# Kernel optimization log

Measured on AMD Instinct MI355X. Metric: run time of the kernel, lower is better.

## Reference

```python
import jax, jax.numpy as jnp
import numpy as np

B, S, D, R, N, K = 4, 2048, 1024, 128, 64, 8

def _orthogonal(key, shape):
    # mimic nn.init.orthogonal_ for a (D, R) matrix, D >= R
    a = jax.random.normal(key, (shape[0], shape[1]), dtype=jnp.float32)
    q, r = jnp.linalg.qr(a)
    q = q * jnp.sign(jnp.diagonal(r))[None, :]
    return q

def setup_inputs() -> dict:
    key = jax.random.key(0)
    kx, kr, kn = jax.random.split(key, 3)
    x = jax.random.normal(kx, (B, S, D), dtype=jnp.float32)
    # router: nn.Linear(d_model, n_compress, bias=False) -> weight [N, D]
    bound = 1.0 / np.sqrt(D)
    router_w = jax.random.uniform(kr, (N, D), minval=-bound, maxval=bound, dtype=jnp.float32)
    # compress_neurons: [N, D, R], each slice orthogonally initialized
    nkeys = jax.random.split(kn, N)
    neurons = jax.vmap(lambda k: _orthogonal(k, (D, R)))(nkeys)  # [N, D, R]
    return {"x": x, "router_w": router_w, "neurons": neurons}

def reference(x, router_w, neurons):
    # scores: [B, S, N]
    scores = jnp.einsum('bsd,nd->bsn', x, router_w)
    topk_scores, topk_idx = jax.lax.top_k(scores, K)           # [B,S,K]
    weights = jax.nn.softmax(topk_scores, axis=-1)             # [B,S,K]
    # Equivalent to gathering per-token [K,D,R] expert matrices then bmm,
    # but computed as dense all-expert projection + gather (no [B,S,K,D,R] blow-up).
    proj_all = jnp.einsum('bsd,ndr->bsnr', x, neurons)         # [B,S,N,R]
    proj = jnp.take_along_axis(proj_all, topk_idx[..., None], axis=2)  # [B,S,K,R]
    output = jnp.sum(proj * weights[..., None], axis=2)        # [B,S,R]
    return output, weights, topk_idx
```

## Files before the change

kernel.cpp:

```cpp
#include <hip/hip_runtime.h>
#include <hip/hip_bf16.h>
#include <stdint.h>

#define NTOK 8192
#define DIM  1024
#define RD   128
#define NEXP 64
#define TOPK 8
#define MAXT 4096
#define NHB  32
#define JM   32

#define W_OFF (NTOK * RD)
#define I_OFF (W_OFF + NTOK * TOPK)

#define CNT_OFF  0
#define LIST_OFF 1024
#define GC_OFF   (LIST_OFF + NEXP * MAXT * 4)
#define BO_OFF   (GC_OFF + NHB * NEXP * 4)
#define NT_OFF   2360320
#define XB_OFF   (NT_OFF + (size_t)NEXP * RD * DIM * 2)
#define PW_OFF   (XB_OFF + (size_t)NTOK * DIM * 2)
#define PW_END   (PW_OFF + (size_t)NTOK * TOPK * RD * 2)

using bh8 = __attribute__((ext_vector_type(8))) short;
using fx4 = __attribute__((ext_vector_type(4))) float;
using dx2 = __attribute__((ext_vector_type(2))) double;
using dx4 = __attribute__((ext_vector_type(4))) double;

__device__ inline unsigned short f2bf(float f) {
    union { __hip_bfloat16 h; unsigned short u; } v;
    v.h = __float2bfloat16(f);
    return v.u;
}

__global__ __launch_bounds__(256) void nt_cast(const float* __restrict__ nr,
                                               __hip_bfloat16* __restrict__ nT) {
    int bx  = blockIdx.x;
    int e   = bx >> 5;
    int sub = bx & 31;
    int d0  = (sub >> 1) * 64;
    int r0  = (sub & 1) * 64;
    __shared__ float t[64][65];
    int tid = threadIdx.x;
    int dd  = tid >> 2;
    int rr4 = (tid & 3) * 16;
    const float* src = nr + ((size_t)e * DIM + d0 + dd) * RD + r0 + rr4;
    fx4 v[4];
    #pragma unroll
    for (int u = 0; u < 4; ++u) v[u] = ((const fx4*)src)[u];
    #pragma unroll
    for (int u = 0; u < 4; ++u)
        #pragma unroll
        for (int c = 0; c < 4; ++c) t[dd][rr4 + u * 4 + c] = v[u][c];
    __syncthreads();
    int rr  = tid >> 2;
    int dd4 = (tid & 3) * 16;
    union { unsigned short u[16]; uint4 q[2]; } o;
    #pragma unroll
    for (int i = 0; i < 16; ++i) o.u[i] = f2bf(t[dd4 + i][rr]);
    __hip_bfloat16* dst = nT + ((size_t)e * RD + r0 + rr) * DIM + d0 + dd4;
    ((uint4*)dst)[0] = o.q[0];
    ((uint4*)dst)[1] = o.q[1];
}

__global__ __launch_bounds__(256) void score_k(const float* __restrict__ x,
                                               const float* __restrict__ rw,
                                               double* __restrict__ sp,
                                               unsigned short* __restrict__ xb) {
    __shared__ __align__(16) char smem[2 * 64 * 66 * 8];
    double (*Xs)[66] = (double (*)[66])smem;
    double (*Ws)[66] = (double (*)[66])(smem + 64 * 66 * 8);
    double (*Ssc)[65] = (double (*)[65])smem;

    int tid = threadIdx.x;
    int ds  = blockIdx.x & 3;
    int tb  = (blockIdx.x >> 2) * 64;
    int ni  = tid & 15;
    int ti  = tid >> 4;

    double acc[4][4];
    #pragma unroll
    for (int i = 0; i < 4; ++i)
        #pragma unroll
        for (int j = 0; j < 4; ++j) acc[i][j] = 0.0;

    int srow = tid >> 2;
    int scol = (tid & 3) * 16;

    fx4 xv[4], wv[4];
    {
        const float* xs = x  + (size_t)(tb + srow) * DIM + ds * 256 + scol;
        const float* ws = rw + (size_t)srow        * DIM + ds * 256 + scol;
        #pragma unroll
        for (int u = 0; u < 4; ++u) { xv[u] = ((const fx4*)xs)[u]; wv[u] = ((const fx4*)ws)[u]; }
    }

    for (int c = 0; c < 4; ++c) {
        __syncthreads();
        #pragma unroll
        for (int u = 0; u < 4; ++u) {
            #pragma unroll
            for (int k = 0; k < 4; k += 2) {
                dx2 xd; xd[0] = (double)xv[u][k]; xd[1] = (double)xv[u][k + 1];
                *(dx2*)&Xs[srow][scol + u * 4 + k] = xd;
                dx2 wd; wd[0] = (double)wv[u][k]; wd[1] = (double)wv[u][k + 1];
                *(dx2*)&Ws[srow][scol + u * 4 + k] = wd;
            }
        }
        {
            bh8 o0, o1;
            #pragma unroll
            for (int c2 = 0; c2 < 4; ++c2) {
                o0[c2]     = (short)f2bf(xv[0][c2]);
                o0[4 + c2] = (short)f2bf(xv[1][c2]);
                o1[c2]     = (short)f2bf(xv[2][c2]);
                o1[4 + c2] = (short)f2bf(xv[3][c2]);
            }
            unsigned short* xd = xb + (size_t)(tb + srow) * DIM + ds * 256 + c * 64 + scol;
            *(bh8*)xd = o0;
            *(bh8*)(xd + 8) = o1;
        }
        __syncthreads();
        if (c < 3) {
            int d0 = ds * 256 + (c + 1) * 64;
            const float* xs = x  + (size_t)(tb + srow) * DIM + d0 + scol;
            const float* ws = rw + (size_t)srow        * DIM + d0 + scol;
            #pragma unroll
            for (int u = 0; u < 4; ++u) { xv[u] = ((const fx4*)xs)[u]; wv[u] = ((const fx4*)ws)[u]; }
        }
        for (int dq = 0; dq < 64; dq += 4) {
            dx4 xa[4], wb[4];
            #pragma unroll
            for (int i = 0; i < 4; ++i) xa[i] = *(const dx4*)&Xs[ti * 4 + i][dq];
            #pragma unroll
            for (int j = 0; j < 4; ++j) wb[j] = *(const dx4*)&Ws[ni + 16 * j][dq];
            #pragma unroll
            for (int i = 0; i < 4; ++i)
                #pragma unroll
                for (int j = 0; j < 4; ++j)
                    acc[i][j] += xa[i][0] * wb[j][0]
                               + xa[i][1] * wb[j][1]
                               + xa[i][2] * wb[j][2]
                               + xa[i][3] * wb[j][3];
        }
    }
    __syncthreads();
    #pragma unroll
    for (int i = 0; i < 4; ++i)
        #pragma unroll
        for (int j = 0; j < 4; ++j) Ssc[ti * 4 + i][ni + 16 * j] = acc[i][j];
    __syncthreads();

    int t  = tid >> 2;
    int n0 = (tid & 3) * 16;
    double* dst = sp + ((size_t)ds * NTOK + tb + t) * NEXP + n0;
    #pragma unroll
    for (int k = 0; k < 16; ++k) dst[k] = Ssc[t][n0 + k];
}

__global__ __launch_bounds__(256) void topk_k(const double* __restrict__ sp,
                                              float* __restrict__ out) {
    int wave = threadIdx.x >> 6, lane = threadIdx.x & 63;
    int T = blockIdx.x * 4 + wave;

    const double* base = sp + (size_t)T * NEXP + lane;
    const size_t SL = (size_t)NTOK * NEXP;
    double s = base[0] + base[SL] + base[2 * SL] + base[3 * SL];

    double vals[TOPK]; int idxs[TOPK];
    double cur = s;
    #pragma unroll
    for (int p = 0; p < TOPK; ++p) {
        double v = cur; int i = lane;
        #pragma unroll
        for (int off = 32; off > 0; off >>= 1) {
            double ov = __shfl_xor(v, off, 64);
            int    oi = __shfl_xor(i, off, 64);
            if (ov > v || (ov == v && oi < i)) { v = ov; i = oi; }
        }
        vals[p] = v; idxs[p] = i;
        if (lane == i) cur = -1e300;
    }

    double m = vals[0], sum = 0.0, ex[TOPK];
    #pragma unroll
    for (int p = 0; p < TOPK; ++p) { ex[p] = exp(vals[p] - m); sum += ex[p]; }
    double inv = 1.0 / sum;

    if (lane < TOPK) {
        int p = lane;
        out[W_OFF + T * TOPK + p] = (float)(ex[p] * inv);
        out[I_OFF + T * TOPK + p] = (float)idxs[p];
    }
}

__global__ __launch_bounds__(256) void hist_k(const float* __restrict__ out,
                                              int* __restrict__ gcnt) {
    __shared__ int lh[NEXP];
    int tid = threadIdx.x;
    if (tid < NEXP) lh[tid] = 0;
    __syncthreads();
    int T = blockIdx.x * 256 + tid;
    const fx4* ip = (const fx4*)(out + I_OFF + (size_t)T * TOPK);
    fx4 a = ip[0], b = ip[1];
    #pragma unroll
    for (int p = 0; p < 4; ++p) { atomicAdd(&lh[(int)a[p]], 1); atomicAdd(&lh[(int)b[p]], 1); }
    __syncthreads();
    if (tid < NEXP) gcnt[blockIdx.x * NEXP + tid] = lh[tid];
}

__global__ __launch_bounds__(64) void scan_k(const int* __restrict__ gcnt,
                                             int* __restrict__ boff,
                                             int* __restrict__ cnt) {
    int e = threadIdx.x;
    int s = 0;
    #pragma unroll
    for (int b = 0; b < NHB; ++b) {
        boff[b * NEXP + e] = e * MAXT + s;
        s += gcnt[b * NEXP + e];
    }
    cnt[e] = s;
}

__global__ __launch_bounds__(256) void scatter_k(const float* __restrict__ out,
                                                 const int* __restrict__ boff,
                                                 int* __restrict__ lists) {
    __shared__ int lh[NEXP];
    __shared__ int bo[NEXP];
    int tid = threadIdx.x;
    if (tid < NEXP) { lh[tid] = 0; bo[tid] = boff[blockIdx.x * NEXP + tid]; }
    __syncthreads();
    int T = blockIdx.x * 256 + tid;
    const fx4* ip = (const fx4*)(out + I_OFF + (size_t)T * TOPK);
    fx4 a = ip[0], b = ip[1];
    int ev[TOPK] = {(int)a[0], (int)a[1], (int)a[2], (int)a[3],
                    (int)b[0], (int)b[1], (int)b[2], (int)b[3]};
    #pragma unroll
    for (int p = 0; p < TOPK; ++p) {
        int e = ev[p];
        int pos = atomicAdd(&lh[e], 1);
        lists[bo[e] + pos] = (T << 3) | p;
    }
}

__global__ __launch_bounds__(256) void gemm_k(const unsigned short* __restrict__ xb,
                                              const unsigned short* __restrict__ nTb,
                                              const int* __restrict__ cnt,
                                              const int* __restrict__ lists,
                                              float* __restrict__ outf,
                                              unsigned short* __restrict__ pw,
                                              int use_pw) {
    int e = blockIdx.x & 63;
    int j = blockIdx.x >> 6;
    int ce = cnt[e];
    int base = j * 64;
    if (base >= ce) return;

    __shared__ unsigned short As[2][64 * 64];
    __shared__ unsigned short Bs[2][128 * 64];
    __shared__ int   plist[64];
    __shared__ float wl[64];

    int tid = threadIdx.x;
    int wave = tid >> 6, lane = tid & 63;
    if (tid < 64) {
        int idx = base + tid;
        int p = (idx < ce) ? lists[e * MAXT + idx] : -1;
        plist[tid] = p;
        wl[tid] = (p >= 0) ? outf[W_OFF + p] : 0.0f;
    }
    __syncthreads();

    fx4 acc[2][4];
    #pragma unroll
    for (int a = 0; a < 2; ++a)
        #pragma unroll
        for (int b = 0; b < 4; ++b) acc[a][b] = (fx4){0.f, 0.f, 0.f, 0.f};

    unsigned soff = 16u * (unsigned)((lane & 7) ^ (lane >> 3));
    const char* asrc[2];
    const char* bsrc[4];
    const char* xbb = (const char*)xb;
    const char* ntb = (const char*)(nTb + (size_t)e * RD * DIM);
    #pragma unroll
    for (int c = 0; c < 2; ++c) {
        int row = (wave * 2 + c) * 8 + (lane >> 3);
        int p = plist[row];
        int tok = (p < 0) ? 0 : (p >> 3);
        asrc[c] = xbb + (size_t)tok * (DIM * 2) + soff;
    }
    #pragma unroll
    for (int c = 0; c < 4; ++c) {
        int row = (wave * 4 + c) * 8 + (lane >> 3);
        bsrc[c] = ntb + (size_t)row * (DIM * 2) + soff;
    }

    int wm = (wave >> 1) * 32, wn = (wave & 1) * 64;
    int lr = lane & 15, lk = (lane >> 4) * 8;
    int lg = lane >> 4;

    auto stage = [&](int kt, int bsel) {
        int db = kt * 128;
        #pragma unroll
        for (int c = 0; c < 2; ++c) {
            __builtin_amdgcn_global_load_lds(
                (const __attribute__((address_space(1))) void*)(asrc[c] + db),
                (__attribute__((address_space(3))) void*)(&As[bsel][(wave * 2 + c) * 512]),
                16, 0, 0);
        }
        #pragma unroll
        for (int c = 0; c < 4; ++c) {
            __builtin_amdgcn_global_load_lds(
                (const __attribute__((address_space(1))) void*)(bsrc[c] + db),
                (__attribute__((address_space(3))) void*)(&Bs[bsel][(wave * 4 + c) * 512]),
                16, 0, 0);
        }
    };

    auto mfma_tile = [&](int bsel) {
        const char* Ab = (const char*)As[bsel];
        const char* Bb = (const char*)Bs[bsel];
        #pragma unroll
        for (int kk = 0; kk < 2; ++kk) {
            int k0 = kk * 32;
            bh8 av[2], bv[4];
            #pragma unroll
            for (int mf = 0; mf < 2; ++mf) {
                unsigned row = (unsigned)(wm + mf * 16 + lr);
                unsigned bo = row * 128 + (unsigned)(k0 + lk) * 2;
                bo ^= (row & 7) << 4;
                av[mf] = *(const bh8*)(Ab + bo);
            }
            #pragma unroll
            for (int nf = 0; nf < 4; ++nf) {
                unsigned row = (unsigned)(wn + nf * 16 + lr);
                unsigned bo = row * 128 + (unsigned)(k0 + lk) * 2;
                bo ^= (row & 7) << 4;
                bv[nf] = *(const bh8*)(Bb + bo);
            }
            #pragma unroll
            for (int mf = 0; mf < 2; ++mf)
                #pragma unroll
                for (int nf = 0; nf < 4; ++nf)
                    acc[mf][nf] = __builtin_amdgcn_mfma_f32_16x16x32_bf16(av[mf], bv[nf], acc[mf][nf], 0, 0, 0);
        }
    };

    stage(0, 0);
    stage(1, 1);

    for (int kt = 0; kt < 15; ++kt) {
        int bsel = kt & 1;
        asm volatile("s_waitcnt vmcnt(6)" ::: "memory");
        __builtin_amdgcn_s_barrier();
        asm volatile("" ::: "memory");
        mfma_tile(bsel);
        asm volatile("s_waitcnt lgkmcnt(0)" ::: "memory");
        __builtin_amdgcn_s_barrier();
        asm volatile("" ::: "memory");
        if (kt < 14) stage(kt + 2, bsel);
    }
    asm volatile("s_waitcnt vmcnt(0)" ::: "memory");
    __builtin_amdgcn_s_barrier();
    asm volatile("" ::: "memory");
    mfma_tile(1);

    if (use_pw) {
        #pragma unroll
        for (int mf = 0; mf < 2; ++mf) {
            #pragma unroll
            for (int rg = 0; rg < 4; ++rg) {
                int row = wm + mf * 16 + lg * 4 + rg;
                int p = plist[row];
                if (p < 0) continue;
                float wg = wl[row];
                #pragma unroll
                for (int nf = 0; nf < 4; ++nf) {
                    int r = wn + nf * 16 + lr;
                    pw[(size_t)p * RD + r] = f2bf(acc[mf][nf][rg] * wg);
                }
            }
        }
    } else {
        #pragma unroll
        for (int mf = 0; mf < 2; ++mf) {
            #pragma unroll
            for (int rg = 0; rg < 4; ++rg) {
                int row = wm + mf * 16 + lg * 4 + rg;
                int p = plist[row];
                if (p < 0) continue;
                float wg = wl[row];
                int t = p >> 3;
                #pragma unroll
                for (int nf = 0; nf < 4; ++nf) {
                    int r = wn + nf * 16 + lr;
                    atomicAdd(&outf[(size_t)t * RD + r], acc[mf][nf][rg] * wg);
                }
            }
        }
    }
}

__global__ __launch_bounds__(256) void reduce_k(const unsigned short* __restrict__ pw,
                                                float* __restrict__ y) {
    int gid = blockIdx.x * 256 + threadIdx.x;
    int t = gid >> 7, r = gid & 127;
    float s = 0.f;
    #pragma unroll
    for (int k = 0; k < TOPK; ++k) {
        unsigned int w = ((unsigned int)pw[((size_t)t * TOPK + k) * RD + r]) << 16;
        s += __uint_as_float(w);
    }
    y[gid] = s;
}

extern "C" void kernel_launch(void* const* d_in, const int* in_sizes, int n_in,
                              void* d_out, int out_size, void* d_ws, size_t ws_size,
                              hipStream_t stream) {
    const float* x  = (const float*)d_in[0];
    const float* rw = (const float*)d_in[1];
    const float* nr = (const float*)d_in[2];
    float* out = (float*)d_out;
    char* ws = (char*)d_ws;
    int*    cnt   = (int*)(ws + CNT_OFF);
    int*    lists = (int*)(ws + LIST_OFF);
    int*    gcnt  = (int*)(ws + GC_OFF);
    int*    boff  = (int*)(ws + BO_OFF);
    __hip_bfloat16* nT = (__hip_bfloat16*)(ws + NT_OFF);
    double* sp    = (double*)(ws + NT_OFF);
    unsigned short* xbu = (unsigned short*)(ws + XB_OFF);
    unsigned short* pw  = (unsigned short*)(ws + PW_OFF);

    const int use_pw = (ws_size >= (size_t)PW_END) ? 1 : 0;

    if (!use_pw)
        hipMemsetAsync(out, 0, (size_t)NTOK * RD * sizeof(float), stream);
    score_k<<<512, 256, 0, stream>>>(x, rw, sp, xbu);
    topk_k<<<NTOK / 4, 256, 0, stream>>>(sp, out);
    nt_cast<<<2048, 256, 0, stream>>>(nr, nT);
    hist_k<<<NHB, 256, 0, stream>>>(out, gcnt);
    scan_k<<<1, 64, 0, stream>>>(gcnt, boff, cnt);
    scatter_k<<<NHB, 256, 0, stream>>>(out, boff, lists);
    gemm_k<<<NEXP * JM, 256, 0, stream>>>(xbu, (const unsigned short*)nT, cnt, lists, out, pw, use_pw);
    if (use_pw)
        reduce_k<<<(NTOK * RD) / 256, 256, 0, stream>>>(pw, out);
}
```

Before: 112.8 us.

## Merge score and weight-cast kernels, fold scan into scatter

When the workspace is large enough, the router-score kernel and the expert-weight bf16 transpose/cast now run as one launch, with block index choosing the role. The score partials move to the per-pair scratch region so they no longer alias the transposed weights. The separate single-block prefix-scan kernel is removed: each scatter block recomputes its own per-expert offsets from the histogram counts, and block 0 writes the totals. Together this removes two launches and lets the cast run alongside scoring. The cost is a larger shared-memory footprint for the cast blocks and a few redundant count reads in every scatter block.

```diff
diff --git a/kernel.cpp b/kernel.cpp
--- a/kernel.cpp
+++ b/kernel.cpp
@@ -17,7 +17,6 @@
 #define CNT_OFF  0
 #define LIST_OFF 1024
 #define GC_OFF   (LIST_OFF + NEXP * MAXT * 4)
-#define BO_OFF   (GC_OFF + NHB * NEXP * 4)
 #define NT_OFF   2360320
 #define XB_OFF   (NT_OFF + (size_t)NEXP * RD * DIM * 2)
 #define PW_OFF   (XB_OFF + (size_t)NTOK * DIM * 2)
@@ -34,15 +33,14 @@
     return v.u;
 }
 
-__global__ __launch_bounds__(256) void nt_cast(const float* __restrict__ nr,
-                                               __hip_bfloat16* __restrict__ nT) {
-    int bx  = blockIdx.x;
+__device__ inline void nt_body(int bx, int tid, char* smemraw,
+                               const float* __restrict__ nr,
+                               __hip_bfloat16* __restrict__ nT) {
+    float (*t)[65] = (float (*)[65])smemraw;
     int e   = bx >> 5;
     int sub = bx & 31;
     int d0  = (sub >> 1) * 64;
     int r0  = (sub & 1) * 64;
-    __shared__ float t[64][65];
-    int tid = threadIdx.x;
     int dd  = tid >> 2;
     int rr4 = (tid & 3) * 16;
     const float* src = nr + ((size_t)e * DIM + d0 + dd) * RD + r0 + rr4;
@@ -64,18 +62,17 @@
     ((uint4*)dst)[1] = o.q[1];
 }
 
-__global__ __launch_bounds__(256) void score_k(const float* __restrict__ x,
-                                               const float* __restrict__ rw,
-                                               double* __restrict__ sp,
-                                               unsigned short* __restrict__ xb) {
-    __shared__ __align__(16) char smem[2 * 64 * 66 * 8];
+__device__ inline void score_body(int bx, int tid, char* smem,
+                                  const float* __restrict__ x,
+                                  const float* __restrict__ rw,
+                                  double* __restrict__ sp,
+                                  unsigned short* __restrict__ xb) {
     double (*Xs)[66] = (double (*)[66])smem;
     double (*Ws)[66] = (double (*)[66])(smem + 64 * 66 * 8);
     double (*Ssc)[65] = (double (*)[65])smem;
 
-    int tid = threadIdx.x;
-    int ds  = blockIdx.x & 3;
-    int tb  = (blockIdx.x >> 2) * 64;
+    int ds  = bx & 3;
+    int tb  = (bx >> 2) * 64;
     int ni  = tid & 15;
     int ti  = tid >> 4;
 
@@ -159,6 +156,31 @@
     for (int k = 0; k < 16; ++k) dst[k] = Ssc[t][n0 + k];
 }
 
+__global__ __launch_bounds__(256) void score_nt_k(const float* __restrict__ x,
+                                                  const float* __restrict__ rw,
+                                                  const float* __restrict__ nr,
+                                                  double* __restrict__ sp,
+                                                  __hip_bfloat16* __restrict__ nT,
+                                                  unsigned short* __restrict__ xb) {
+    __shared__ __align__(16) char smem[2 * 64 * 66 * 8];
+    int tid = threadIdx.x;
+    if (blockIdx.x < 512) score_body(blockIdx.x, tid, smem, x, rw, sp, xb);
+    else                  nt_body(blockIdx.x - 512, tid, smem, nr, nT);
+}
+
+__global__ __launch_bounds__(256) void score_k(const float* __restrict__ x,
+                                               const float* __restrict__ rw,
+                                               double* __restrict__ sp,
+                                               unsigned short* __restrict__ xb) {
+    __shared__ __align__(16) char smem[2 * 64 * 66 * 8];
+    score_body(blockIdx.x, threadIdx.x, smem, x, rw, sp, xb);
+}
+__global__ __launch_bounds__(256) void nt_cast(const float* __restrict__ nr,
+                                               __hip_bfloat16* __restrict__ nT) {
+    __shared__ __align__(16) char smem[64 * 65 * 4];
+    nt_body(blockIdx.x, threadIdx.x, smem, nr, nT);
+}
+
 __global__ __launch_bounds__(256) void topk_k(const double* __restrict__ sp,
                                               float* __restrict__ out) {
     int wave = threadIdx.x >> 6, lane = threadIdx.x & 63;
@@ -210,26 +232,25 @@
     if (tid < NEXP) gcnt[blockIdx.x * NEXP + tid] = lh[tid];
 }
 
-__global__ __launch_bounds__(64) void scan_k(const int* __restrict__ gcnt,
-                                             int* __restrict__ boff,
-                                             int* __restrict__ cnt) {
-    int e = threadIdx.x;
-    int s = 0;
-    #pragma unroll
-    for (int b = 0; b < NHB; ++b) {
-        boff[b * NEXP + e] = e * MAXT + s;
-        s += gcnt[b * NEXP + e];
-    }
-    cnt[e] = s;
-}
-
 __global__ __launch_bounds__(256) void scatter_k(const float* __restrict__ out,
-                                                 const int* __restrict__ boff,
-                                                 int* __restrict__ lists) {
+                                                 const int* __restrict__ gcnt,
+                                                 int* __restrict__ lists,
+                                                 int* __restrict__ cnt) {
     __shared__ int lh[NEXP];
     __shared__ int bo[NEXP];
     int tid = threadIdx.x;
-    if (tid < NEXP) { lh[tid] = 0; bo[tid] = boff[blockIdx.x * NEXP + tid]; }
+    if (tid < NEXP) {
+        lh[tid] = 0;
+        int s = 0, tot = 0;
+        #pragma unroll
+        for (int b = 0; b < NHB; ++b) {
+            int g = gcnt[b * NEXP + tid];
+            if (b < (int)blockIdx.x) s += g;
+            tot += g;
+        }
+        bo[tid] = tid * MAXT + s;
+        if (blockIdx.x == 0) cnt[tid] = tot;
+    }
     __syncthreads();
     int T = blockIdx.x * 256 + tid;
     const fx4* ip = (const fx4*)(out + I_OFF + (size_t)T * TOPK);
@@ -426,23 +447,28 @@
     int*    cnt   = (int*)(ws + CNT_OFF);
     int*    lists = (int*)(ws + LIST_OFF);
     int*    gcnt  = (int*)(ws + GC_OFF);
-    int*    boff  = (int*)(ws + BO_OFF);
     __hip_bfloat16* nT = (__hip_bfloat16*)(ws + NT_OFF);
-    double* sp    = (double*)(ws + NT_OFF);
     unsigned short* xbu = (unsigned short*)(ws + XB_OFF);
     unsigned short* pw  = (unsigned short*)(ws + PW_OFF);
 
     const int use_pw = (ws_size >= (size_t)PW_END) ? 1 : 0;
 
-    if (!use_pw)
+    if (use_pw) {
+        double* sp = (double*)(ws + PW_OFF);
+        score_nt_k<<<512 + 2048, 256, 0, stream>>>(x, rw, nr, sp, nT, xbu);
+        topk_k<<<NTOK / 4, 256, 0, stream>>>(sp, out);
+        hist_k<<<NHB, 256, 0, stream>>>(out, gcnt);
+        scatter_k<<<NHB, 256, 0, stream>>>(out, gcnt, lists, cnt);
+        gemm_k<<<NEXP * JM, 256, 0, stream>>>(xbu, (const unsigned short*)nT, cnt, lists, out, pw, 1);
+        reduce_k<<<(NTOK * RD) / 256, 256, 0, stream>>>(pw, out);
+    } else {
+        double* sp = (double*)(ws + NT_OFF);
         hipMemsetAsync(out, 0, (size_t)NTOK * RD * sizeof(float), stream);
-    score_k<<<512, 256, 0, stream>>>(x, rw, sp, xbu);
-    topk_k<<<NTOK / 4, 256, 0, stream>>>(sp, out);
-    nt_cast<<<2048, 256, 0, stream>>>(nr, nT);
-    hist_k<<<NHB, 256, 0, stream>>>(out, gcnt);
-    scan_k<<<1, 64, 0, stream>>>(gcnt, boff, cnt);
-    scatter_k<<<NHB, 256, 0, stream>>>(out, boff, lists);
-    gemm_k<<<NEXP * JM, 256, 0, stream>>>(xbu, (const unsigned short*)nT, cnt, lists, out, pw, use_pw);
-    if (use_pw)
-        reduce_k<<<(NTOK * RD) / 256, 256, 0, stream>>>(pw, out);
-}
+        score_k<<<512, 256, 0, stream>>>(x, rw, sp, xbu);
+        topk_k<<<NTOK / 4, 256, 0, stream>>>(sp, out);
+        nt_cast<<<2048, 256, 0, stream>>>(nr, nT);
+        hist_k<<<NHB, 256, 0, stream>>>(out, gcnt);
+        scatter_k<<<NHB, 256, 0, stream>>>(out, gcnt, lists, cnt);
+        gemm_k<<<NEXP * JM, 256, 0, stream>>>(xbu, (const unsigned short*)nT, cnt, lists, out, pw, 0);
+    }
+}
```

Result: slower. 140.2 us (+24.3%).

## Halve score tile to 32 tokens and fold prefix scan into scatter

Applied to the files above, without the earlier changes.

The fp64 router score kernel now processes 32 tokens per block instead of 64, doubling the grid to 1024 blocks and cutting shared memory and accumulator registers per thread. This should improve occupancy and load balance across CUs. Separately, the single-block scan kernel is removed: each scatter block computes its own exclusive prefix over the per-block histograms, and block 0 writes the totals. That saves one launch and a dependency step, but each block re-reads the whole histogram array, and the W tile is now reloaded for every 32 tokens.

```diff
diff --git a/kernel.cpp b/kernel.cpp
--- a/kernel.cpp
+++ b/kernel.cpp
@@ -17,7 +17,6 @@
 #define CNT_OFF  0
 #define LIST_OFF 1024
 #define GC_OFF   (LIST_OFF + NEXP * MAXT * 4)
-#define BO_OFF   (GC_OFF + NHB * NEXP * 4)
 #define NT_OFF   2360320
 #define XB_OFF   (NT_OFF + (size_t)NEXP * RD * DIM * 2)
 #define PW_OFF   (XB_OFF + (size_t)NTOK * DIM * 2)
@@ -68,75 +67,81 @@
                                                const float* __restrict__ rw,
                                                double* __restrict__ sp,
                                                unsigned short* __restrict__ xb) {
-    __shared__ __align__(16) char smem[2 * 64 * 66 * 8];
+    __shared__ __align__(16) char smem[32 * 66 * 8 + 64 * 66 * 8];
     double (*Xs)[66] = (double (*)[66])smem;
-    double (*Ws)[66] = (double (*)[66])(smem + 64 * 66 * 8);
+    double (*Ws)[66] = (double (*)[66])(smem + 32 * 66 * 8);
     double (*Ssc)[65] = (double (*)[65])smem;
 
     int tid = threadIdx.x;
     int ds  = blockIdx.x & 3;
-    int tb  = (blockIdx.x >> 2) * 64;
+    int tb  = (blockIdx.x >> 2) * 32;
     int ni  = tid & 15;
     int ti  = tid >> 4;
 
-    double acc[4][4];
-    #pragma unroll
-    for (int i = 0; i < 4; ++i)
+    double acc[2][4];
+    #pragma unroll
+    for (int i = 0; i < 2; ++i)
         #pragma unroll
         for (int j = 0; j < 4; ++j) acc[i][j] = 0.0;
 
-    int srow = tid >> 2;
-    int scol = (tid & 3) * 16;
-
-    fx4 xv[4], wv[4];
+    int sxr = tid >> 3;
+    int sxc = (tid & 7) * 8;
+    int swr = tid >> 2;
+    int swc = (tid & 3) * 16;
+
+    fx4 xv[2], wv[4];
     {
-        const float* xs = x  + (size_t)(tb + srow) * DIM + ds * 256 + scol;
-        const float* ws = rw + (size_t)srow        * DIM + ds * 256 + scol;
-        #pragma unroll
-        for (int u = 0; u < 4; ++u) { xv[u] = ((const fx4*)xs)[u]; wv[u] = ((const fx4*)ws)[u]; }
+        const float* xs = x  + (size_t)(tb + sxr) * DIM + ds * 256 + sxc;
+        const float* ws = rw + (size_t)swr        * DIM + ds * 256 + swc;
+        xv[0] = ((const fx4*)xs)[0]; xv[1] = ((const fx4*)xs)[1];
+        #pragma unroll
+        for (int u = 0; u < 4; ++u) wv[u] = ((const fx4*)ws)[u];
     }
 
     for (int c = 0; c < 4; ++c) {
         __syncthreads();
         #pragma unroll
-        for (int u = 0; u < 4; ++u) {
+        for (int u = 0; u < 2; ++u) {
             #pragma unroll
             for (int k = 0; k < 4; k += 2) {
                 dx2 xd; xd[0] = (double)xv[u][k]; xd[1] = (double)xv[u][k + 1];
-                *(dx2*)&Xs[srow][scol + u * 4 + k] = xd;
+                *(dx2*)&Xs[sxr][sxc + u * 4 + k] = xd;
+            }
+        }
+        #pragma unroll
+        for (int u = 0; u < 4; ++u) {
+            #pragma unroll
+            for (int k = 0; k < 4; k += 2) {
                 dx2 wd; wd[0] = (double)wv[u][k]; wd[1] = (double)wv[u][k + 1];
-                *(dx2*)&Ws[srow][scol + u * 4 + k] = wd;
+                *(dx2*)&Ws[swr][swc + u * 4 + k] = wd;
             }
         }
         {
-            bh8 o0, o1;
+            bh8 o;
             #pragma unroll
             for (int c2 = 0; c2 < 4; ++c2) {
-                o0[c2]     = (short)f2bf(xv[0][c2]);
-                o0[4 + c2] = (short)f2bf(xv[1][c2]);
-                o1[c2]     = (short)f2bf(xv[2][c2]);
-                o1[4 + c2] = (short)f2bf(xv[3][c2]);
-            }
-            unsigned short* xd = xb + (size_t)(tb + srow) * DIM + ds * 256 + c * 64 + scol;
-            *(bh8*)xd = o0;
-            *(bh8*)(xd + 8) = o1;
+                o[c2]     = (short)f2bf(xv[0][c2]);
+                o[4 + c2] = (short)f2bf(xv[1][c2]);
+            }
+            *(bh8*)(xb + (size_t)(tb + sxr) * DIM + ds * 256 + c * 64 + sxc) = o;
         }
         __syncthreads();
         if (c < 3) {
             int d0 = ds * 256 + (c + 1) * 64;
-            const float* xs = x  + (size_t)(tb + srow) * DIM + d0 + scol;
-            const float* ws = rw + (size_t)srow        * DIM + d0 + scol;
-            #pragma unroll
-            for (int u = 0; u < 4; ++u) { xv[u] = ((const fx4*)xs)[u]; wv[u] = ((const fx4*)ws)[u]; }
+            const float* xs = x  + (size_t)(tb + sxr) * DIM + d0 + sxc;
+            const float* ws = rw + (size_t)swr        * DIM + d0 + swc;
+            xv[0] = ((const fx4*)xs)[0]; xv[1] = ((const fx4*)xs)[1];
+            #pragma unroll
+            for (int u = 0; u < 4; ++u) wv[u] = ((const fx4*)ws)[u];
         }
         for (int dq = 0; dq < 64; dq += 4) {
-            dx4 xa[4], wb[4];
-            #pragma unroll
-            for (int i = 0; i < 4; ++i) xa[i] = *(const dx4*)&Xs[ti * 4 + i][dq];
+            dx4 xa[2], wb[4];
+            #pragma unroll
+            for (int i = 0; i < 2; ++i) xa[i] = *(const dx4*)&Xs[ti * 2 + i][dq];
             #pragma unroll
             for (int j = 0; j < 4; ++j) wb[j] = *(const dx4*)&Ws[ni + 16 * j][dq];
             #pragma unroll
-            for (int i = 0; i < 4; ++i)
+            for (int i = 0; i < 2; ++i)
                 #pragma unroll
                 for (int j = 0; j < 4; ++j)
                     acc[i][j] += xa[i][0] * wb[j][0]
@@ -147,16 +152,16 @@
     }
     __syncthreads();
     #pragma unroll
-    for (int i = 0; i < 4; ++i)
-        #pragma unroll
-        for (int j = 0; j < 4; ++j) Ssc[ti * 4 + i][ni + 16 * j] = acc[i][j];
-    __syncthreads();
-
-    int t  = tid >> 2;
-    int n0 = (tid & 3) * 16;
+    for (int i = 0; i < 2; ++i)
+        #pragma unroll
+        for (int j = 0; j < 4; ++j) Ssc[ti * 2 + i][ni + 16 * j] = acc[i][j];
+    __syncthreads();
+
+    int t  = tid >> 3;
+    int n0 = (tid & 7) * 8;
     double* dst = sp + ((size_t)ds * NTOK + tb + t) * NEXP + n0;
     #pragma unroll
-    for (int k = 0; k < 16; ++k) dst[k] = Ssc[t][n0 + k];
+    for (int k = 0; k < 8; ++k) dst[k] = Ssc[t][n0 + k];
 }
 
 __global__ __launch_bounds__(256) void topk_k(const double* __restrict__ sp,
@@ -210,26 +215,25 @@
     if (tid < NEXP) gcnt[blockIdx.x * NEXP + tid] = lh[tid];
 }
 
-__global__ __launch_bounds__(64) void scan_k(const int* __restrict__ gcnt,
-                                             int* __restrict__ boff,
-                                             int* __restrict__ cnt) {
-    int e = threadIdx.x;
-    int s = 0;
-    #pragma unroll
-    for (int b = 0; b < NHB; ++b) {
-        boff[b * NEXP + e] = e * MAXT + s;
-        s += gcnt[b * NEXP + e];
-    }
-    cnt[e] = s;
-}
-
 __global__ __launch_bounds__(256) void scatter_k(const float* __restrict__ out,
-                                                 const int* __restrict__ boff,
-                                                 int* __restrict__ lists) {
+                                                 const int* __restrict__ gcnt,
+                                                 int* __restrict__ lists,
+                                                 int* __restrict__ cnt) {
     __shared__ int lh[NEXP];
     __shared__ int bo[NEXP];
     int tid = threadIdx.x;
-    if (tid < NEXP) { lh[tid] = 0; bo[tid] = boff[blockIdx.x * NEXP + tid]; }
+    if (tid < NEXP) {
+        lh[tid] = 0;
+        int s = 0, tot = 0;
+        #pragma unroll
+        for (int b = 0; b < NHB; ++b) {
+            int g = gcnt[b * NEXP + tid];
+            if (b < (int)blockIdx.x) s += g;
+            tot += g;
+        }
+        bo[tid] = tid * MAXT + s;
+        if (blockIdx.x == 0) cnt[tid] = tot;
+    }
     __syncthreads();
     int T = blockIdx.x * 256 + tid;
     const fx4* ip = (const fx4*)(out + I_OFF + (size_t)T * TOPK);
@@ -426,7 +430,6 @@
     int*    cnt   = (int*)(ws + CNT_OFF);
     int*    lists = (int*)(ws + LIST_OFF);
     int*    gcnt  = (int*)(ws + GC_OFF);
-    int*    boff  = (int*)(ws + BO_OFF);
     __hip_bfloat16* nT = (__hip_bfloat16*)(ws + NT_OFF);
     double* sp    = (double*)(ws + NT_OFF);
     unsigned short* xbu = (unsigned short*)(ws + XB_OFF);
@@ -436,12 +439,11 @@
 
     if (!use_pw)
         hipMemsetAsync(out, 0, (size_t)NTOK * RD * sizeof(float), stream);
-    score_k<<<512, 256, 0, stream>>>(x, rw, sp, xbu);
+    score_k<<<1024, 256, 0, stream>>>(x, rw, sp, xbu);
     topk_k<<<NTOK / 4, 256, 0, stream>>>(sp, out);
     nt_cast<<<2048, 256, 0, stream>>>(nr, nT);
     hist_k<<<NHB, 256, 0, stream>>>(out, gcnt);
-    scan_k<<<1, 64, 0, stream>>>(gcnt, boff, cnt);
-    scatter_k<<<NHB, 256, 0, stream>>>(out, boff, lists);
+    scatter_k<<<NHB, 256, 0, stream>>>(out, gcnt, lists, cnt);
     gemm_k<<<NEXP * JM, 256, 0, stream>>>(xbu, (const unsigned short*)nT, cnt, lists, out, pw, use_pw);
     if (use_pw)
         reduce_k<<<(NTOK * RD) / 256, 256, 0, stream>>>(pw, out);
```

New measurement: 114.0 us. No clear change (+1.1%).
